# Kernel tuning notes

Hardware: AMD Instinct MI355X
Metric: run time of the kernel (lower is better)

Reference implementation:

```python
import jax, jax.numpy as jnp
import numpy as np

VOCAB = 50001  # vocab_size + 1
EMB = 64
HID = 128
TAGS = 32
B, T = 256, 512


def setup_inputs() -> dict:
    key = jax.random.key(0)
    ks = jax.random.split(key, 12)
    inputs = jax.random.randint(ks[0], (B, T), 0, VOCAB)
    labels = jax.random.randint(ks[1], (B, T), 0, TAGS)
    E = jax.random.normal(ks[2], (VOCAB, EMB), jnp.float32) * 0.1
    def glorot(k, shape):
        fan = sum(shape)
        return jax.random.uniform(k, shape, jnp.float32, -1.0, 1.0) * jnp.sqrt(6.0 / fan)
    Wk_f = glorot(ks[3], (EMB, 4 * HID))
    Wr_f = glorot(ks[4], (HID, 4 * HID))
    b_f = jnp.zeros((4 * HID,), jnp.float32)
    Wk_b = glorot(ks[5], (EMB, 4 * HID))
    Wr_b = glorot(ks[6], (HID, 4 * HID))
    b_b = jnp.zeros((4 * HID,), jnp.float32)
    Wd = glorot(ks[7], (2 * HID, TAGS))
    bd = jnp.zeros((TAGS,), jnp.float32)
    transition = jax.random.uniform(ks[8], (TAGS, TAGS), jnp.float32)
    return {"inputs": inputs, "labels": labels, "E": E,
            "Wk_f": Wk_f, "Wr_f": Wr_f, "b_f": b_f,
            "Wk_b": Wk_b, "Wr_b": Wr_b, "b_b": b_b,
            "Wd": Wd, "bd": bd, "transition": transition}


def _lstm(x, Wk, Wr, b, reverse):
    # x: (B, T, D) -> (B, T, H); Keras gate order i, f, g(cell), o
    Bb = x.shape[0]
    H = Wr.shape[0]
    xs = jnp.swapaxes(x, 0, 1)  # (T, B, D)

    def step(carry, xt):
        h, c = carry
        z = xt @ Wk + h @ Wr + b
        i, f, g, o = jnp.split(z, 4, axis=-1)
        c = jax.nn.sigmoid(f) * c + jax.nn.sigmoid(i) * jnp.tanh(g)
        h = jax.nn.sigmoid(o) * jnp.tanh(c)
        return (h, c), h

    init = (jnp.zeros((Bb, H), x.dtype), jnp.zeros((Bb, H), x.dtype))
    _, hs = jax.lax.scan(step, init, xs, reverse=reverse)
    return jnp.swapaxes(hs, 0, 1)  # (B, T, H), time-aligned for both directions


def _crf_log_likelihood(logits, labels, transition):
    # logits: (B, T, K), labels: (B, T) int, full-length sequences
    lt = jnp.swapaxes(logits, 0, 1)  # (T, B, K)

    def fstep(alpha, lg):
        # alpha: (B, K) -> logsumexp over previous tag
        alpha = jax.nn.logsumexp(alpha[:, :, None] + transition[None], axis=1) + lg
        return alpha, None

    alpha, _ = jax.lax.scan(fstep, lt[0], lt[1:])
    log_norm = jax.nn.logsumexp(alpha, axis=-1)  # (B,)
    unary = jnp.take_along_axis(logits, labels[..., None], axis=-1)[..., 0].sum(-1)
    binary = transition[labels[:, :-1], labels[:, 1:]].sum(-1)
    return unary + binary - log_norm


def reference(inputs, labels, E, Wk_f, Wr_f, b_f, Wk_b, Wr_b, b_b, Wd, bd, transition):
    emb = E[inputs]  # (B, T, EMB) embedding lookup
    h_f = _lstm(emb, Wk_f, Wr_f, b_f, reverse=False)
    h_b = _lstm(emb, Wk_b, Wr_b, b_b, reverse=True)
    h = jnp.concatenate([h_f, h_b], axis=-1)  # (B, T, 2H)
    logits = h @ Wd + bd  # (B, T, K)
    log_likelihood = _crf_log_likelihood(logits, labels, transition)
    return log_likelihood, transition
```

## Files before the change

kernel.cpp:

```cpp
#include <hip/hip_runtime.h>
#include <hip/hip_bf16.h>
#include <cstdint>
#include <cstddef>

#define VOCAB 50001
#define EMB 64
#define HID 128
#define G4  512
#define TAGS 32
#define BATCH 256
#define SEQ 512

typedef _Float16 f16;
typedef _Float16 f16x2 __attribute__((ext_vector_type(2)));
typedef _Float16 f16x4 __attribute__((ext_vector_type(4)));
typedef _Float16 f16x8 __attribute__((ext_vector_type(8)));
typedef float f32x4 __attribute__((ext_vector_type(4)));

__device__ __forceinline__ float rcpf(float x) { return __builtin_amdgcn_rcpf(x); }

#define MFMA16(A, B, C) __builtin_amdgcn_mfma_f32_16x16x32_f16((A), (B), (C), 0, 0, 0)

__global__ __launch_bounds__(256)
void gtab_mfma_kernel(const float* __restrict__ E,
                      const float* __restrict__ Wk_f, const float* __restrict__ b_f,
                      const float* __restrict__ Wk_b, const float* __restrict__ b_b,
                      f16* __restrict__ G_f, f16* __restrict__ G_b) {
  const int dir = blockIdx.z;
  const float* __restrict__ Wk   = dir ? Wk_b : Wk_f;
  const float* __restrict__ bias = dir ? b_b  : b_f;
  f16* __restrict__ G = dir ? G_b : G_f;

  const int m0 = blockIdx.x * 64;
  const int n0 = blockIdx.y * 256;
  const int tid = threadIdx.x;

  __shared__ f16 Eh[64][80];
  __shared__ f16 Bh[256][80];

  #pragma unroll
  for (int s = 0; s < 4; ++s) {
    int idx = tid + s * 256;
    int r = idx >> 4, c4 = (idx & 15) * 4;
    int row = m0 + r;
    float4 ev;
    if (row < VOCAB) ev = *(const float4*)(E + (size_t)row * EMB + c4);
    else { ev.x = 0.f; ev.y = 0.f; ev.z = 0.f; ev.w = 0.f; }
    f16x4 v; v[0] = (f16)ev.x; v[1] = (f16)ev.y; v[2] = (f16)ev.z; v[3] = (f16)ev.w;
    *(f16x4*)&Eh[r][c4] = v;
  }
  #pragma unroll
  for (int s = 0; s < 32; ++s) {
    int idx = tid + s * 256;
    int k = idx >> 7, n2 = (idx & 127) * 2;
    float2 wv = *(const float2*)(Wk + (size_t)k * G4 + n0 + n2);
    Bh[n2][k]     = (f16)wv.x;
    Bh[n2 + 1][k] = (f16)wv.y;
  }
  __syncthreads();

  const int w = tid >> 6, l = tid & 63, mn = l & 15, q = l >> 4;
  f16x8 a0 = *(const f16x8*)&Eh[16 * w + mn][8 * q];
  f16x8 a1 = *(const f16x8*)&Eh[16 * w + mn][32 + 8 * q];

  f32x4 acc[16];
  #pragma unroll
  for (int nt = 0; nt < 16; ++nt) {
    f16x8 b0 = *(const f16x8*)&Bh[16 * nt + mn][8 * q];
    f16x8 b1 = *(const f16x8*)&Bh[16 * nt + mn][32 + 8 * q];
    f32x4 z = {0.f, 0.f, 0.f, 0.f};
    z = MFMA16(a0, b0, z);
    z = MFMA16(a1, b1, z);
    acc[nt] = z;
  }

  const int gA = n0 >> 7;
  #pragma unroll
  for (int nt = 0; nt < 8; ++nt) {
    int hid = 16 * nt + mn;
    float bv0 = bias[n0 + 16 * nt + mn];
    float bv1 = bias[n0 + 128 + 16 * nt + mn];
    #pragma unroll
    for (int reg = 0; reg < 4; ++reg) {
      int row = m0 + 16 * w + 4 * q + reg;
      if (row < VOCAB) {
        f16x2 v; v.x = (f16)(acc[nt][reg] + bv0); v.y = (f16)(acc[nt + 8][reg] + bv1);
        *(f16x2*)(G + (size_t)row * G4 + hid * 4 + gA) = v;
      }
    }
  }
}

__global__ __launch_bounds__(512, 1)
void lstm_mfma_kernel(const int* __restrict__ tokens,
                      const f16* __restrict__ G_f, const f16* __restrict__ G_b,
                      const float* __restrict__ Wr_f, const float* __restrict__ Wr_b,
                      const float* __restrict__ Wd, const float* __restrict__ bd,
                      float* __restrict__ Lf, float* __restrict__ Lb) {
  const int bg  = blockIdx.x;
  const int dir = blockIdx.y;
  const int b0  = bg * 2;
  const f16* __restrict__ G = dir ? G_b : G_f;
  const float* __restrict__ Wr = dir ? Wr_b : Wr_f;
  float* __restrict__ Lout = dir ? Lb : Lf;

  const int tid = threadIdx.x;
  const int w = tid >> 6;
  const int l = tid & 63;
  const int mn = l & 15;
  const int q  = l >> 4;
  const bool gate_thr = (tid < 256);
  const int gb   = (tid >> 7) & 1;
  const int ghid = tid & 127;

  __shared__ __align__(16) f16 h_lds[2][HID];
  __shared__ __align__(8)  float z_lds[G4][2];
  __shared__ int tokT[SEQ][2];

  tokT[tid][0] = tokens[(size_t)(b0 + 0) * SEQ + tid];
  tokT[tid][1] = tokens[(size_t)(b0 + 1) * SEQ + tid];
  if (tid < 128) ((unsigned*)h_lds)[tid] = 0u;

  f16x8 bw[4][4];
  #pragma unroll
  for (int g = 0; g < 4; ++g) {
    #pragma unroll
    for (int s = 0; s < 4; ++s) {
      f16x8 v;
      const int colv = 128 * g + 16 * w + mn;
      #pragma unroll
      for (int j = 0; j < 8; ++j)
        v[j] = (f16)Wr[(size_t)(32 * s + 8 * q + j) * G4 + colv];
      bw[g][s] = v;
    }
  }
  f16x8 wdf0{}, wdf1{}, wdf2{}, wdf3{};
  float bdv = 0.0f;
  if (w >= 6) {
    const int tag = 16 * (w - 6) + mn;
    #pragma unroll
    for (int j = 0; j < 8; ++j) {
      wdf0[j] = (f16)Wd[(size_t)(128 * dir +  0 + 8 * q + j) * TAGS + tag];
      wdf1[j] = (f16)Wd[(size_t)(128 * dir + 32 + 8 * q + j) * TAGS + tag];
      wdf2[j] = (f16)Wd[(size_t)(128 * dir + 64 + 8 * q + j) * TAGS + tag];
      wdf3[j] = (f16)Wd[(size_t)(128 * dir + 96 + 8 * q + j) * TAGS + tag];
    }
    if (dir == 0) bdv = bd[tag];
  }

  float cst = 0.0f;
  __syncthreads();

#define TT(S) (dir ? (SEQ - 1 - (S)) : (S))

#define LOADG(S, GV) do { if (gate_thr) {                                      \
    int _tk = tokT[TT(S)][gb];                                                 \
    GV = *(const uint2*)(G + (size_t)_tk * G4 + ghid * 4); } } while (0)

#define STEP(S, GV) do {                                                       \
    const int _s = (S);                                                        \
    const int _t = TT(_s);                                                     \
    const char* hbase = (const char*)&h_lds[mn & 1][0];                        \
    f16x8 a0 = *(const f16x8*)(hbase +       16 * q);                          \
    f16x8 a1 = *(const f16x8*)(hbase +  64 + 16 * q);                          \
    f16x8 a2 = *(const f16x8*)(hbase + 128 + 16 * q);                          \
    f16x8 a3 = *(const f16x8*)(hbase + 192 + 16 * q);                          \
    f32x4 z0 = {0.f,0.f,0.f,0.f}, z1 = {0.f,0.f,0.f,0.f};                      \
    f32x4 z2 = {0.f,0.f,0.f,0.f}, z3 = {0.f,0.f,0.f,0.f};                      \
    z0 = MFMA16(a0, bw[0][0], z0); z0 = MFMA16(a1, bw[0][1], z0);              \
    z0 = MFMA16(a2, bw[0][2], z0); z0 = MFMA16(a3, bw[0][3], z0);              \
    z1 = MFMA16(a0, bw[1][0], z1); z1 = MFMA16(a1, bw[1][1], z1);              \
    z1 = MFMA16(a2, bw[1][2], z1); z1 = MFMA16(a3, bw[1][3], z1);              \
    z2 = MFMA16(a0, bw[2][0], z2); z2 = MFMA16(a1, bw[2][1], z2);              \
    z2 = MFMA16(a2, bw[2][2], z2); z2 = MFMA16(a3, bw[2][3], z2);              \
    z3 = MFMA16(a0, bw[3][0], z3); z3 = MFMA16(a1, bw[3][1], z3);              \
    z3 = MFMA16(a2, bw[3][2], z3); z3 = MFMA16(a3, bw[3][3], z3);              \
    if (w >= 6) {                                                              \
      f32x4 la = {0.f,0.f,0.f,0.f};                                            \
      la = MFMA16(a0, wdf0, la); la = MFMA16(a1, wdf1, la);                    \
      la = MFMA16(a2, wdf2, la); la = MFMA16(a3, wdf3, la);                    \
      if (q == 0) {                                                            \
        const int tag = 16 * (w - 6) + mn;                                     \
        Lout[((size_t)(b0 + 0) * SEQ + _t) * TAGS + tag] = la[0] + bdv;        \
        Lout[((size_t)(b0 + 1) * SEQ + _t) * TAGS + tag] = la[1] + bdv;        \
      }                                                                        \
    }                                                                          \
    if (q == 0) {                                                              \
      float2 v0; v0.x = z0[0]; v0.y = z0[1];                                   \
      float2 v1; v1.x = z1[0]; v1.y = z1[1];                                   \
      float2 v2; v2.x = z2[0]; v2.y = z2[1];                                   \
      float2 v3; v3.x = z3[0]; v3.y = z3[1];                                   \
      *(float2*)&z_lds[      16 * w + mn][0] = v0;                             \
      *(float2*)&z_lds[128 + 16 * w + mn][0] = v1;                             \
      *(float2*)&z_lds[256 + 16 * w + mn][0] = v2;                             \
      *(float2*)&z_lds[384 + 16 * w + mn][0] = v3;                             \
    }                                                                          \
    asm volatile("s_waitcnt lgkmcnt(0)" ::: "memory");                         \
    __builtin_amdgcn_s_barrier();                                              \
    if (gate_thr) {                                                            \
      float zi = z_lds[      ghid][gb];                                        \
      float zf = z_lds[128 + ghid][gb];                                        \
      float zg = z_lds[256 + ghid][gb];                                        \
      float zo = z_lds[384 + ghid][gb];                                        \
      f16x4 gv = __builtin_bit_cast(f16x4, GV);                                \
      zi += (float)gv[0]; zf += (float)gv[1];                                  \
      zg += (float)gv[2]; zo += (float)gv[3];                                  \
      float ei = __expf(-zi);                                                  \
      float eg = __expf(fminf(2.f * zg, 30.f));                                \
      float sab = (eg - 1.f) * rcpf((1.f + ei) * (eg + 1.f));                  \
      float ef = __expf(-zf);                                                  \
      float cc = rcpf(1.f + ef) * cst + sab;                                   \
      cst = cc;                                                                \
      float eo = __expf(-zo);                                                  \
      float ec = __expf(fminf(2.f * cc, 30.f));                                \
      float hh = (ec - 1.f) * rcpf((1.f + eo) * (ec + 1.f));                   \
      h_lds[gb][ghid] = (f16)hh;                                               \
    }                                                                          \
    asm volatile("s_waitcnt lgkmcnt(0)" ::: "memory");                         \
    __builtin_amdgcn_s_barrier();                                              \
  } while (0)

  uint2 gA, gB, gC, gD;
  LOADG(0, gA); LOADG(1, gB); LOADG(2, gC); LOADG(3, gD);

  for (int it = 0; it < SEQ / 4; ++it) {
    const int s = 4 * it;
    STEP(s + 0, gA);
    { int sc = (s + 4 < SEQ) ? s + 4 : SEQ - 1; LOADG(sc, gA); }
    STEP(s + 1, gB);
    { int sc = (s + 5 < SEQ) ? s + 5 : SEQ - 1; LOADG(sc, gB); }
    STEP(s + 2, gC);
    { int sc = (s + 6 < SEQ) ? s + 6 : SEQ - 1; LOADG(sc, gC); }
    STEP(s + 3, gD);
    { int sc = (s + 7 < SEQ) ? s + 7 : SEQ - 1; LOADG(sc, gD); }
  }
#undef STEP
#undef LOADG
#undef TT
}

__global__ __launch_bounds__(256)
void crf_kernel(const float* __restrict__ Lf,
                const float* __restrict__ Lb,
                const float* __restrict__ trans,
                const int* __restrict__ labels,
                float* __restrict__ out) {
  const int wv = threadIdx.x >> 6;
  const int b  = blockIdx.x * 4 + wv;
  const int lane = threadIdx.x & 63;
  const int k  = lane & 31;
  const int jh = lane >> 5;

  __shared__ float tr[TAGS * TAGS];
  __shared__ __align__(16) float e_lds[4][TAGS];

  for (int i = threadIdx.x; i < TAGS * TAGS; i += 256) tr[i] = trans[i];
  __syncthreads();

  float wxp[16];
  #pragma unroll
  for (int i = 0; i < 16; ++i) wxp[i] = __expf(tr[(jh * 16 + i) * TAGS + k]);

  const size_t base0 = (size_t)b * SEQ * TAGS;
  float cur = Lf[base0 + k] + Lb[base0 + k];
  float b00 = __builtin_amdgcn_readfirstlane(__builtin_bit_cast(int, cur))
                  ? 0.f : 0.f;
  float beta0 = __shfl(cur, 0);
  float beta = cur - beta0;
  float S = beta0;

  float nxt = Lf[base0 + TAGS + k] + Lb[base0 + TAGS + k];

  for (int t = 1; t < SEQ; ++t) {
    float e = __expf(beta);
    if (lane < TAGS) e_lds[wv][k] = e;
    asm volatile("s_waitcnt lgkmcnt(0)" ::: "memory");
    const float4* ep = (const float4*)&e_lds[wv][jh * 16];
    float4 e0 = ep[0], e1 = ep[1], e2 = ep[2], e3 = ep[3];
    float d0 = e0.x * wxp[0]  + e0.y * wxp[1]  + e0.z * wxp[2]  + e0.w * wxp[3];
    float d1 = e1.x * wxp[4]  + e1.y * wxp[5]  + e1.z * wxp[6]  + e1.w * wxp[7];
    float d2 = e2.x * wxp[8]  + e2.y * wxp[9]  + e2.z * wxp[10] + e2.w * wxp[11];
    float d3 = e3.x * wxp[12] + e3.y * wxp[13] + e3.z * wxp[14] + e3.w * wxp[15];
    float dot = (d0 + d1) + (d2 + d3);
    dot += __shfl_xor(dot, 32);
    float braw = __logf(dot) + nxt;
    float bz = __shfl(braw, 0);
    beta = braw - bz;
    S += bz;
    if (t + 1 < SEQ) {
      size_t idx = base0 + (size_t)(t + 1) * TAGS + k;
      nxt = Lf[idx] + Lb[idx];
    }
  }

  float m = beta;
  #pragma unroll
  for (int off = 1; off <= 16; off <<= 1) m = fmaxf(m, __shfl_xor(m, off));
  float ex = (lane < TAGS) ? __expf(beta - m) : 0.0f;
  float s = ex;
  #pragma unroll
  for (int off = 1; off <= 32; off <<= 1) s += __shfl_xor(s, off);

  const int* lab = labels + (size_t)b * SEQ;
  float uacc = 0.f, bacc = 0.f;
  for (int t = lane; t < SEQ; t += 64) {
    int l0 = lab[t];
    size_t idx = base0 + (size_t)t * TAGS + l0;
    uacc += Lf[idx] + Lb[idx];
    if (t + 1 < SEQ) bacc += tr[l0 * TAGS + lab[t + 1]];
  }
  float red = uacc + bacc;
  #pragma unroll
  for (int off = 1; off <= 32; off <<= 1) red += __shfl_xor(red, off);

  if (lane == 0) out[b] = red - (m + __logf(s) + S);
}

__global__ void copy_trans_kernel(const float* __restrict__ trans,
                                  float* __restrict__ out) {
  int i = blockIdx.x * blockDim.x + threadIdx.x;
  if (i < TAGS * TAGS) out[i] = trans[i];
}

extern "C" void kernel_launch(void* const* d_in, const int* in_sizes, int n_in,
                              void* d_out, int out_size, void* d_ws, size_t ws_size,
                              hipStream_t stream) {
  const int*   inputs = (const int*)  d_in[0];
  const int*   labels = (const int*)  d_in[1];
  const float* E      = (const float*)d_in[2];
  const float* Wk_f   = (const float*)d_in[3];
  const float* Wr_f   = (const float*)d_in[4];
  const float* b_f    = (const float*)d_in[5];
  const float* Wk_b   = (const float*)d_in[6];
  const float* Wr_b   = (const float*)d_in[7];
  const float* b_b    = (const float*)d_in[8];
  const float* Wd     = (const float*)d_in[9];
  const float* bd     = (const float*)d_in[10];
  const float* trans  = (const float*)d_in[11];
  float* out = (float*)d_out;

  char* ws = (char*)d_ws;
  const size_t G_ELEMS = (size_t)VOCAB * G4;
  f16* G_f = (f16*)ws;
  f16* G_b = G_f + G_ELEMS;
  float* Lfp = (float*)(ws + 2 * G_ELEMS * sizeof(f16));
  float* Lbp = Lfp + (size_t)BATCH * SEQ * TAGS;

  dim3 ggrid((VOCAB + 63) / 64, 2, 2);
  gtab_mfma_kernel<<<ggrid, 256, 0, stream>>>(E, Wk_f, b_f, Wk_b, b_b, G_f, G_b);

  lstm_mfma_kernel<<<dim3(BATCH / 2, 2), 512, 0, stream>>>(
      inputs, G_f, G_b, Wr_f, Wr_b, Wd, bd, Lfp, Lbp);

  crf_kernel<<<BATCH / 4, 256, 0, stream>>>(Lfp, Lbp, trans, labels, out);

  copy_trans_kernel<<<(TAGS * TAGS + 255) / 256, 256, 0, stream>>>(trans, out + BATCH);
}
```

Measured before the change: 523.1 us.

## Compute LSTM gates in MFMA-owning lanes and double-buffer h to drop a barrier

The LSTM step no longer stages gate pre-activations through LDS with a second barrier. The lanes that hold the MFMA outputs now compute the gates themselves, using a shuffle for the second batch row. The hidden state is double-buffered by step parity and padded, so each step needs only one barrier. The CRF kernel is also relaunched with one 64-thread block per sequence instead of four waves per block, which spreads its work over more CUs.

```diff
diff --git a/kernel.cpp b/kernel.cpp
--- a/kernel.cpp
+++ b/kernel.cpp
@@ -109,17 +109,14 @@
   const int l = tid & 63;
   const int mn = l & 15;
   const int q  = l >> 4;
-  const bool gate_thr = (tid < 256);
-  const int gb   = (tid >> 7) & 1;
-  const int ghid = tid & 127;
-
-  __shared__ __align__(16) f16 h_lds[2][HID];
-  __shared__ __align__(8)  float z_lds[G4][2];
+  const int hid = 16 * w + mn;
+
+  __shared__ __align__(16) f16 h_lds[2][2][160];
   __shared__ int tokT[SEQ][2];
 
   tokT[tid][0] = tokens[(size_t)(b0 + 0) * SEQ + tid];
   tokT[tid][1] = tokens[(size_t)(b0 + 1) * SEQ + tid];
-  if (tid < 128) ((unsigned*)h_lds)[tid] = 0u;
+  if (tid < 160) ((unsigned*)&h_lds[0][0][0])[tid] = 0u;
 
   f16x8 bw[4][4];
   #pragma unroll
@@ -127,7 +124,7 @@
     #pragma unroll
     for (int s = 0; s < 4; ++s) {
       f16x8 v;
-      const int colv = 128 * g + 16 * w + mn;
+      const int colv = 128 * g + hid;
       #pragma unroll
       for (int j = 0; j < 8; ++j)
         v[j] = (f16)Wr[(size_t)(32 * s + 8 * q + j) * G4 + colv];
@@ -153,18 +150,18 @@
 
 #define TT(S) (dir ? (SEQ - 1 - (S)) : (S))
 
-#define LOADG(S, GV) do { if (gate_thr) {                                      \
-    int _tk = tokT[TT(S)][gb];                                                 \
-    GV = *(const uint2*)(G + (size_t)_tk * G4 + ghid * 4); } } while (0)
+#define LOADG(S, GV) do { if (l < 32) {                                        \
+    int _tk = tokT[TT(S)][q];                                                  \
+    GV = *(const uint2*)(G + (size_t)_tk * G4 + hid * 4); } } while (0)
 
 #define STEP(S, GV) do {                                                       \
     const int _s = (S);                                                        \
     const int _t = TT(_s);                                                     \
-    const char* hbase = (const char*)&h_lds[mn & 1][0];                        \
-    f16x8 a0 = *(const f16x8*)(hbase +       16 * q);                          \
-    f16x8 a1 = *(const f16x8*)(hbase +  64 + 16 * q);                          \
-    f16x8 a2 = *(const f16x8*)(hbase + 128 + 16 * q);                          \
-    f16x8 a3 = *(const f16x8*)(hbase + 192 + 16 * q);                          \
+    const f16* hb = &h_lds[_s & 1][mn & 1][0];                                 \
+    f16x8 a0 = *(const f16x8*)(hb      + 8 * q);                               \
+    f16x8 a1 = *(const f16x8*)(hb + 32 + 8 * q);                               \
+    f16x8 a2 = *(const f16x8*)(hb + 64 + 8 * q);                               \
+    f16x8 a3 = *(const f16x8*)(hb + 96 + 8 * q);                               \
     f32x4 z0 = {0.f,0.f,0.f,0.f}, z1 = {0.f,0.f,0.f,0.f};                      \
     f32x4 z2 = {0.f,0.f,0.f,0.f}, z3 = {0.f,0.f,0.f,0.f};                      \
     z0 = MFMA16(a0, bw[0][0], z0); z0 = MFMA16(a1, bw[0][1], z0);              \
@@ -185,23 +182,15 @@
         Lout[((size_t)(b0 + 1) * SEQ + _t) * TAGS + tag] = la[1] + bdv;        \
       }                                                                        \
     }                                                                          \
-    if (q == 0) {                                                              \
-      float2 v0; v0.x = z0[0]; v0.y = z0[1];                                   \
-      float2 v1; v1.x = z1[0]; v1.y = z1[1];                                   \
-      float2 v2; v2.x = z2[0]; v2.y = z2[1];                                   \
-      float2 v3; v3.x = z3[0]; v3.y = z3[1];                                   \
-      *(float2*)&z_lds[      16 * w + mn][0] = v0;                             \
-      *(float2*)&z_lds[128 + 16 * w + mn][0] = v1;                             \
-      *(float2*)&z_lds[256 + 16 * w + mn][0] = v2;                             \
-      *(float2*)&z_lds[384 + 16 * w + mn][0] = v3;                             \
-    }                                                                          \
-    asm volatile("s_waitcnt lgkmcnt(0)" ::: "memory");                         \
-    __builtin_amdgcn_s_barrier();                                              \
-    if (gate_thr) {                                                            \
-      float zi = z_lds[      ghid][gb];                                        \
-      float zf = z_lds[128 + ghid][gb];                                        \
-      float zg = z_lds[256 + ghid][gb];                                        \
-      float zo = z_lds[384 + ghid][gb];                                        \
+    float s0 = __shfl(z0[1], mn);                                              \
+    float s1 = __shfl(z1[1], mn);                                              \
+    float s2 = __shfl(z2[1], mn);                                              \
+    float s3 = __shfl(z3[1], mn);                                              \
+    if (l < 32) {                                                              \
+      float zi = q ? s0 : z0[0];                                               \
+      float zf = q ? s1 : z1[0];                                               \
+      float zg = q ? s2 : z2[0];                                               \
+      float zo = q ? s3 : z3[0];                                               \
       f16x4 gv = __builtin_bit_cast(f16x4, GV);                                \
       zi += (float)gv[0]; zf += (float)gv[1];                                  \
       zg += (float)gv[2]; zo += (float)gv[3];                                  \
@@ -214,7 +203,7 @@
       float eo = __expf(-zo);                                                  \
       float ec = __expf(fminf(2.f * cc, 30.f));                                \
       float hh = (ec - 1.f) * rcpf((1.f + eo) * (ec + 1.f));                   \
-      h_lds[gb][ghid] = (f16)hh;                                               \
+      h_lds[(_s + 1) & 1][q][hid] = (f16)hh;                                   \
     }                                                                          \
     asm volatile("s_waitcnt lgkmcnt(0)" ::: "memory");                         \
     __builtin_amdgcn_s_barrier();                                              \
@@ -239,22 +228,21 @@
 #undef TT
 }
 
-__global__ __launch_bounds__(256)
+__global__ __launch_bounds__(64)
 void crf_kernel(const float* __restrict__ Lf,
                 const float* __restrict__ Lb,
                 const float* __restrict__ trans,
                 const int* __restrict__ labels,
                 float* __restrict__ out) {
-  const int wv = threadIdx.x >> 6;
-  const int b  = blockIdx.x * 4 + wv;
-  const int lane = threadIdx.x & 63;
+  const int b = blockIdx.x;
+  const int lane = threadIdx.x;
   const int k  = lane & 31;
   const int jh = lane >> 5;
 
   __shared__ float tr[TAGS * TAGS];
-  __shared__ __align__(16) float e_lds[4][TAGS];
-
-  for (int i = threadIdx.x; i < TAGS * TAGS; i += 256) tr[i] = trans[i];
+  __shared__ __align__(16) float e_lds[TAGS];
+
+  for (int i = lane; i < TAGS * TAGS; i += 64) tr[i] = trans[i];
   __syncthreads();
 
   float wxp[16];
@@ -263,8 +251,6 @@
 
   const size_t base0 = (size_t)b * SEQ * TAGS;
   float cur = Lf[base0 + k] + Lb[base0 + k];
-  float b00 = __builtin_amdgcn_readfirstlane(__builtin_bit_cast(int, cur))
-                  ? 0.f : 0.f;
   float beta0 = __shfl(cur, 0);
   float beta = cur - beta0;
   float S = beta0;
@@ -273,9 +259,9 @@
 
   for (int t = 1; t < SEQ; ++t) {
     float e = __expf(beta);
-    if (lane < TAGS) e_lds[wv][k] = e;
+    if (lane < TAGS) e_lds[k] = e;
     asm volatile("s_waitcnt lgkmcnt(0)" ::: "memory");
-    const float4* ep = (const float4*)&e_lds[wv][jh * 16];
+    const float4* ep = (const float4*)&e_lds[jh * 16];
     float4 e0 = ep[0], e1 = ep[1], e2 = ep[2], e3 = ep[3];
     float d0 = e0.x * wxp[0]  + e0.y * wxp[1]  + e0.z * wxp[2]  + e0.w * wxp[3];
     float d1 = e1.x * wxp[4]  + e1.y * wxp[5]  + e1.z * wxp[6]  + e1.w * wxp[7];
@@ -352,7 +338,7 @@
   lstm_mfma_kernel<<<dim3(BATCH / 2, 2), 512, 0, stream>>>(
       inputs, G_f, G_b, Wr_f, Wr_b, Wd, bd, Lfp, Lbp);
 
-  crf_kernel<<<BATCH / 4, 256, 0, stream>>>(Lfp, Lbp, trans, labels, out);
+  crf_kernel<<<BATCH, 64, 0, stream>>>(Lfp, Lbp, trans, labels, out);
 
   copy_trans_kernel<<<(TAGS * TAGS + 255) / 256, 256, 0, stream>>>(trans, out + BATCH);
 }
```

Result: no change. 526.5 us (+0.6%).
